# Kernel tuning notes

Measured on AMD Instinct MI355X. Metric: run time of the kernel, lower is better.

Reference implementation:

```python
import jax, jax.numpy as jnp
import numpy as np

B, M, D = 32768, 4096, 128


def setup_inputs() -> dict:
    key = jax.random.key(0)
    k1, k2 = jax.random.split(key)
    local_stats = jax.random.normal(k1, (B, D), dtype=jnp.float32)
    memory = jax.random.normal(k2, (M, D), dtype=jnp.float32)
    return {"local_stats": local_stats, "memory": memory}


def reference(local_stats, memory):
    # attention logits: [B, M] = x @ memory^T (unscaled single-head attention read)
    logits = jnp.einsum("bd,md->bm", local_stats, memory)
    attn = jax.nn.softmax(logits, axis=1)          # [B, M]
    global_stats = jnp.einsum("bm,md->bd", attn, memory)  # [B, D]
    return global_stats
```

## Files before the change

kernel.cpp:

```cpp
#include <hip/hip_runtime.h>
#include <hip/hip_bf16.h>
#include <stdint.h>


typedef float    f32x16 __attribute__((ext_vector_type(16)));
typedef _Float16 f16x8  __attribute__((ext_vector_type(8)));
typedef uint32_t u32;

#define AS1 __attribute__((address_space(1)))
#define AS3 __attribute__((address_space(3)))

#define D_DIM 128
#define B_ROWS 32768
#define TILE_HW 8192
#define HALF_TILES 64

#if __has_builtin(__builtin_amdgcn_exp2f)
#define EXP2F(x) __builtin_amdgcn_exp2f(x)
#else
#define EXP2F(x) exp2f(x)
#endif

__device__ __forceinline__ uint16_t f32_to_f16_bits(float x) {
    _Float16 h = (_Float16)x;
    uint16_t r; __builtin_memcpy(&r, &h, 2);
    return r;
}

__global__ void prep_frags(const float* __restrict__ mem,
                           uint16_t* __restrict__ kv) {
    int t = blockIdx.x * blockDim.x + threadIdx.x;
    int lane = t & 63;
    int fi = t >> 6;
    int f8 = fi & 7, mt = fi >> 3;
    size_t base = (size_t)mt * TILE_HW;
    {
        int m  = mt * 32 + (lane & 31);
        int d0 = f8 * 16 + (lane >> 5) * 8;
        const float* src = mem + (size_t)m * D_DIM + d0;
        #pragma unroll
        for (int e = 0; e < 8; ++e)
            kv[base + f8 * 512 + lane * 8 + e] = f32_to_f16_bits(src[e]);
    }
    {
        int dt = fi & 3, ks = (fi >> 2) & 1;
        int d  = dt * 32 + (lane & 31);
        int m0 = mt * 32 + ks * 16 + (lane >> 5) * 8;
        #pragma unroll
        for (int e = 0; e < 8; ++e)
            kv[base + 4096 + f8 * 512 + lane * 8 + e] =
                f32_to_f16_bits(mem[(size_t)(m0 + e) * D_DIM + d]);
    }
}


#define STAGE(t_, wb_) do {                                                   \
    const char* g_ = (const char*)(kv + (size_t)(tilebase + (t_)) * TILE_HW); \
    char* l_ = (char*)&sbuf[wb_][0];                                          \
    _Pragma("unroll")                                                         \
    for (int j_ = 0; j_ < 4; ++j_) {                                          \
        int ch_ = wave * 4 + j_;                                              \
        __builtin_amdgcn_global_load_lds(                                     \
            (const AS1 char*)(g_ + ch_ * 1024 + lane * 16),                   \
            (AS3 char*)(l_ + ch_ * 1024), 16, 0, 0);                          \
    }                                                                         \
} while (0)

#define MFMA_F16(a_, b_, c_) __builtin_amdgcn_mfma_f32_32x32x16_f16(a_, b_, c_, 0, 0, 0)

#define PSTORE_TILE(Ot_, t_) do {                                             \
    _Pragma("unroll")                                                         \
    for (int g_ = 0; g_ < 4; ++g_) {                                          \
        float4 v_ = { Ot_[4*g_+0], Ot_[4*g_+1], Ot_[4*g_+2], Ot_[4*g_+3] };   \
        int d_ = (t_) * 32 + 8 * g_ + 4 * hi32;                               \
        *(float4*)(prow + d_) = v_;                                           \
    }                                                                         \
} while (0)

__global__ __launch_bounds__(256, 2)
void attn_main(const float* __restrict__ qin,
               const uint16_t* __restrict__ kv,
               float* __restrict__ out0,
               float* __restrict__ pout1,
               float2* __restrict__ pml) {
    __shared__ uint16_t sbuf[2][TILE_HW];

    const int lane = threadIdx.x & 63;
    const int wave = threadIdx.x >> 6;
    const int half = blockIdx.x & 1;
    const int tilebase = half * HALF_TILES;
    const int q0   = (blockIdx.x >> 1) * 128 + wave * 32;
    const int qrow = q0 + (lane & 31);
    const int hi32 = lane >> 5;

    f16x8 qh[8];
    {
        const float LOG2E = 1.44269504088896340736f;
        #pragma unroll
        for (int kk = 0; kk < 8; ++kk) {
            const float* src = qin + (size_t)qrow * D_DIM + kk * 16 + hi32 * 8;
            float4 a = *(const float4*)(src);
            float4 b = *(const float4*)(src + 4);
            float xs[8] = {a.x, a.y, a.z, a.w, b.x, b.y, b.z, b.w};
            #pragma unroll
            for (int e = 0; e < 8; ++e)
                qh[kk][e] = (_Float16)(xs[e] * LOG2E);
        }
    }

    f32x16 O0, O1, O2, O3;
    #pragma unroll
    for (int i = 0; i < 16; ++i) { O0[i]=0.f; O1[i]=0.f; O2[i]=0.f; O3[i]=0.f; }
    float m_run = -1e30f, l_run = 0.f;

    STAGE(0, 0);
    __syncthreads();

    #pragma unroll 1
    for (int t = 0; t < HALF_TILES; ++t) {
        const int rb = t & 1;
        if (t + 1 < HALF_TILES) STAGE(t + 1, rb ^ 1);
        const uint16_t* bp = &sbuf[rb][0] + lane * 8;

        f16x8 kh[8];
        #pragma unroll
        for (int kk = 0; kk < 8; ++kk)
            kh[kk] = *(const f16x8*)(bp + kk * 512);

        f32x16 sA, sB;
        #pragma unroll
        for (int i = 0; i < 16; ++i) { sA[i] = 0.f; sB[i] = 0.f; }
        __builtin_amdgcn_s_setprio(1);
        sA = MFMA_F16(kh[0], qh[0], sA);
        sB = MFMA_F16(kh[1], qh[1], sB);
        sA = MFMA_F16(kh[2], qh[2], sA);
        sB = MFMA_F16(kh[3], qh[3], sB);
        sA = MFMA_F16(kh[4], qh[4], sA);
        sB = MFMA_F16(kh[5], qh[5], sB);
        sA = MFMA_F16(kh[6], qh[6], sA);
        sB = MFMA_F16(kh[7], qh[7], sB);
        __builtin_amdgcn_s_setprio(0);
        f32x16 s = sA + sB;

        {
            float a0=fmaxf(s[0],s[1]),  a1=fmaxf(s[2],s[3]);
            float a2=fmaxf(s[4],s[5]),  a3=fmaxf(s[6],s[7]);
            float a4=fmaxf(s[8],s[9]),  a5=fmaxf(s[10],s[11]);
            float a6=fmaxf(s[12],s[13]),a7=fmaxf(s[14],s[15]);
            float tmax = fmaxf(fmaxf(fmaxf(a0,a1),fmaxf(a2,a3)),
                               fmaxf(fmaxf(a4,a5),fmaxf(a6,a7)));
            tmax = fmaxf(tmax, __shfl_xor(tmax, 32));
            if (__any(tmax > m_run + 8.0f)) {
                float mn = fmaxf(m_run, tmax);
                float fr = EXP2F(m_run - mn);
                m_run = mn; l_run *= fr;
                #pragma unroll
                for (int r = 0; r < 16; ++r) {
                    O0[r] *= fr; O1[r] *= fr; O2[r] *= fr; O3[r] *= fr;
                }
            }
        }
        #pragma unroll
        for (int r = 0; r < 16; ++r) s[r] = EXP2F(s[r] - m_run);
        {
            float q0s=s[0]+s[1],  q1s=s[2]+s[3],  q2s=s[4]+s[5],  q3s=s[6]+s[7];
            float q4s=s[8]+s[9],  q5s=s[10]+s[11],q6s=s[12]+s[13],q7s=s[14]+s[15];
            l_run += ((q0s+q1s)+(q2s+q3s)) + ((q4s+q5s)+(q6s+q7s));
        }

        u32 c_[8];
        #pragma unroll
        for (int j = 0; j < 8; ++j)
            asm("v_cvt_pkrtz_f16_f32 %0, %1, %2"
                : "=v"(c_[j]) : "v"(s[2*j]), "v"(s[2*j+1]));
        asm("v_permlane32_swap_b32 %0, %1" : "+v"(c_[0]), "+v"(c_[2]));
        asm("v_permlane32_swap_b32 %0, %1" : "+v"(c_[1]), "+v"(c_[3]));
        asm("v_permlane32_swap_b32 %0, %1" : "+v"(c_[4]), "+v"(c_[6]));
        asm("v_permlane32_swap_b32 %0, %1" : "+v"(c_[5]), "+v"(c_[7]));
        f16x8 pf0, pf1;
        { u32 w[4] = {c_[0], c_[1], c_[2], c_[3]}; __builtin_memcpy(&pf0, w, 16); }
        { u32 w[4] = {c_[4], c_[5], c_[6], c_[7]}; __builtin_memcpy(&pf1, w, 16); }

        f16x8 vf[8];
        #pragma unroll
        for (int f = 0; f < 8; ++f)
            vf[f] = *(const f16x8*)(bp + 4096 + f * 512);
        __builtin_amdgcn_s_setprio(1);
        O0 = MFMA_F16(vf[0], pf0, O0);
        O1 = MFMA_F16(vf[1], pf0, O1);
        O2 = MFMA_F16(vf[2], pf0, O2);
        O3 = MFMA_F16(vf[3], pf0, O3);
        O0 = MFMA_F16(vf[4], pf1, O0);
        O1 = MFMA_F16(vf[5], pf1, O1);
        O2 = MFMA_F16(vf[6], pf1, O2);
        O3 = MFMA_F16(vf[7], pf1, O3);
        __builtin_amdgcn_s_setprio(0);
        __syncthreads();
    }

    l_run += __shfl_xor(l_run, 32);
    float* prow = (half == 0 ? out0 : pout1) + (size_t)qrow * D_DIM;
    PSTORE_TILE(O0, 0); PSTORE_TILE(O1, 1);
    PSTORE_TILE(O2, 2); PSTORE_TILE(O3, 3);
    if (lane < 32) {
        pml[(size_t)half * B_ROWS + qrow] = make_float2(m_run, l_run);
    }
}

__global__ __launch_bounds__(256)
void merge_halves(const float* __restrict__ pout1,
                  const float2* __restrict__ pml,
                  float* __restrict__ out) {
    int idx  = blockIdx.x * 256 + threadIdx.x;
    int row  = idx >> 5;
    int c4   = idx & 31;
    float2 a = pml[row];
    float2 b = pml[B_ROWS + row];
    float mn = fmaxf(a.x, b.x);
    float wa = EXP2F(a.x - mn);
    float wb = EXP2F(b.x - mn);
    float rinv = 1.0f / (a.y * wa + b.y * wb);
    float4* O = (float4*)(out + (size_t)row * D_DIM) + c4;
    const float4* P1 = (const float4*)(pout1 + (size_t)row * D_DIM) + c4;
    float4 p0 = *O, p1 = *P1;
    float4 v;
    v.x = (p0.x * wa + p1.x * wb) * rinv;
    v.y = (p0.y * wa + p1.y * wb) * rinv;
    v.z = (p0.z * wa + p1.z * wb) * rinv;
    v.w = (p0.w * wa + p1.w * wb) * rinv;
    *O = v;
}

extern "C" void kernel_launch(void* const* d_in, const int* in_sizes, int n_in,
                              void* d_out, int out_size, void* d_ws, size_t ws_size,
                              hipStream_t stream) {
    const float* local_stats = (const float*)d_in[0];
    const float* memory      = (const float*)d_in[1];
    float* out = (float*)d_out;

    uint16_t* kv   = (uint16_t*)d_ws;
    float*   pout1 = (float*)((char*)d_ws + 2 * 1024 * 1024);
    float2*  pml   = (float2*)((char*)pout1 + (size_t)B_ROWS * D_DIM * 4);

    prep_frags<<<256, 256, 0, stream>>>(memory, kv);
    attn_main<<<512, 256, 0, stream>>>(local_stats, kv, out, pout1, pml);
    merge_halves<<<4096, 256, 0, stream>>>(pout1, pml, out);
}
```

Before: 104.1 us.

## Process two KV tiles per iteration with a four-buffer LDS ring

New measurement: 101.4 us. 1.03x faster.

```diff
diff --git a/kernel.cpp b/kernel.cpp
--- a/kernel.cpp
+++ b/kernel.cpp
@@ -68,6 +68,73 @@
 
 #define MFMA_F16(a_, b_, c_) __builtin_amdgcn_mfma_f32_32x32x16_f16(a_, b_, c_, 0, 0, 0)
 
+#define QK(bp_, s_) do {                                                      \
+    f16x8 kh_[8];                                                             \
+    _Pragma("unroll")                                                         \
+    for (int kk_ = 0; kk_ < 8; ++kk_)                                         \
+        kh_[kk_] = *(const f16x8*)((bp_) + kk_ * 512);                        \
+    f32x16 sA_, sB_;                                                          \
+    _Pragma("unroll")                                                         \
+    for (int i_ = 0; i_ < 16; ++i_) { sA_[i_] = 0.f; sB_[i_] = 0.f; }         \
+    sA_ = MFMA_F16(kh_[0], qh[0], sA_);                                       \
+    sB_ = MFMA_F16(kh_[1], qh[1], sB_);                                       \
+    sA_ = MFMA_F16(kh_[2], qh[2], sA_);                                       \
+    sB_ = MFMA_F16(kh_[3], qh[3], sB_);                                       \
+    sA_ = MFMA_F16(kh_[4], qh[4], sA_);                                       \
+    sB_ = MFMA_F16(kh_[5], qh[5], sB_);                                       \
+    sA_ = MFMA_F16(kh_[6], qh[6], sA_);                                       \
+    sB_ = MFMA_F16(kh_[7], qh[7], sB_);                                       \
+    s_ = sA_ + sB_;                                                           \
+} while (0)
+
+#define SMX_PV(s_, bp_) do {                                                  \
+    float a0=fmaxf(s_[0],s_[1]),  a1=fmaxf(s_[2],s_[3]);                      \
+    float a2=fmaxf(s_[4],s_[5]),  a3=fmaxf(s_[6],s_[7]);                      \
+    float a4=fmaxf(s_[8],s_[9]),  a5=fmaxf(s_[10],s_[11]);                    \
+    float a6=fmaxf(s_[12],s_[13]),a7=fmaxf(s_[14],s_[15]);                    \
+    float tmax = fmaxf(fmaxf(fmaxf(a0,a1),fmaxf(a2,a3)),                      \
+                       fmaxf(fmaxf(a4,a5),fmaxf(a6,a7)));                     \
+    tmax = fmaxf(tmax, __shfl_xor(tmax, 32));                                 \
+    if (__any(tmax > m_run + 8.0f)) {                    \
+        float mn = fmaxf(m_run, tmax);                                        \
+        float fr = EXP2F(m_run - mn);                                         \
+        m_run = mn; l_run *= fr;                                              \
+        _Pragma("unroll")                                                     \
+        for (int r_ = 0; r_ < 16; ++r_) {                                     \
+            O0[r_] *= fr; O1[r_] *= fr; O2[r_] *= fr; O3[r_] *= fr;           \
+        }                                                                     \
+    }                                                                         \
+    _Pragma("unroll")                                                         \
+    for (int r_ = 0; r_ < 16; ++r_) s_[r_] = EXP2F(s_[r_] - m_run);           \
+    { float q0s=s_[0]+s_[1],  q1s=s_[2]+s_[3],  q2s=s_[4]+s_[5],  q3s=s_[6]+s_[7];   \
+      float q4s=s_[8]+s_[9],  q5s=s_[10]+s_[11],q6s=s_[12]+s_[13],q7s=s_[14]+s_[15]; \
+      l_run += ((q0s+q1s)+(q2s+q3s)) + ((q4s+q5s)+(q6s+q7s)); }               \
+    u32 c_[8];                                                                \
+    _Pragma("unroll")                                                         \
+    for (int j_ = 0; j_ < 8; ++j_)                                            \
+        asm("v_cvt_pkrtz_f16_f32 %0, %1, %2"                                  \
+            : "=v"(c_[j_]) : "v"(s_[2*j_]), "v"(s_[2*j_+1]));                 \
+    asm("v_permlane32_swap_b32 %0, %1" : "+v"(c_[0]), "+v"(c_[2]));           \
+    asm("v_permlane32_swap_b32 %0, %1" : "+v"(c_[1]), "+v"(c_[3]));           \
+    asm("v_permlane32_swap_b32 %0, %1" : "+v"(c_[4]), "+v"(c_[6]));           \
+    asm("v_permlane32_swap_b32 %0, %1" : "+v"(c_[5]), "+v"(c_[7]));           \
+    f16x8 pf0_, pf1_;                                                         \
+    { u32 w_[4] = {c_[0], c_[1], c_[2], c_[3]}; __builtin_memcpy(&pf0_, w_, 16); } \
+    { u32 w_[4] = {c_[4], c_[5], c_[6], c_[7]}; __builtin_memcpy(&pf1_, w_, 16); } \
+    f16x8 vf_[8];                                                             \
+    _Pragma("unroll")                                                         \
+    for (int f_ = 0; f_ < 8; ++f_)                                            \
+        vf_[f_] = *(const f16x8*)((bp_) + 4096 + f_ * 512);                   \
+    O0 = MFMA_F16(vf_[0], pf0_, O0);                                          \
+    O1 = MFMA_F16(vf_[1], pf0_, O1);                                          \
+    O2 = MFMA_F16(vf_[2], pf0_, O2);                                          \
+    O3 = MFMA_F16(vf_[3], pf0_, O3);                                          \
+    O0 = MFMA_F16(vf_[4], pf1_, O0);                                          \
+    O1 = MFMA_F16(vf_[5], pf1_, O1);                                          \
+    O2 = MFMA_F16(vf_[6], pf1_, O2);                                          \
+    O3 = MFMA_F16(vf_[7], pf1_, O3);                                          \
+} while (0)
+
 #define PSTORE_TILE(Ot_, t_) do {                                             \
     _Pragma("unroll")                                                         \
     for (int g_ = 0; g_ < 4; ++g_) {                                          \
@@ -83,7 +150,7 @@
                float* __restrict__ out0,
                float* __restrict__ pout1,
                float2* __restrict__ pml) {
-    __shared__ uint16_t sbuf[2][TILE_HW];
+    __shared__ uint16_t sbuf[4][TILE_HW];
 
     const int lane = threadIdx.x & 63;
     const int wave = threadIdx.x >> 6;
@@ -114,87 +181,21 @@
     float m_run = -1e30f, l_run = 0.f;
 
     STAGE(0, 0);
+    STAGE(1, 1);
     __syncthreads();
 
     #pragma unroll 1
-    for (int t = 0; t < HALF_TILES; ++t) {
-        const int rb = t & 1;
-        if (t + 1 < HALF_TILES) STAGE(t + 1, rb ^ 1);
-        const uint16_t* bp = &sbuf[rb][0] + lane * 8;
-
-        f16x8 kh[8];
-        #pragma unroll
-        for (int kk = 0; kk < 8; ++kk)
-            kh[kk] = *(const f16x8*)(bp + kk * 512);
-
-        f32x16 sA, sB;
-        #pragma unroll
-        for (int i = 0; i < 16; ++i) { sA[i] = 0.f; sB[i] = 0.f; }
-        __builtin_amdgcn_s_setprio(1);
-        sA = MFMA_F16(kh[0], qh[0], sA);
-        sB = MFMA_F16(kh[1], qh[1], sB);
-        sA = MFMA_F16(kh[2], qh[2], sA);
-        sB = MFMA_F16(kh[3], qh[3], sB);
-        sA = MFMA_F16(kh[4], qh[4], sA);
-        sB = MFMA_F16(kh[5], qh[5], sB);
-        sA = MFMA_F16(kh[6], qh[6], sA);
-        sB = MFMA_F16(kh[7], qh[7], sB);
-        __builtin_amdgcn_s_setprio(0);
-        f32x16 s = sA + sB;
-
-        {
-            float a0=fmaxf(s[0],s[1]),  a1=fmaxf(s[2],s[3]);
-            float a2=fmaxf(s[4],s[5]),  a3=fmaxf(s[6],s[7]);
-            float a4=fmaxf(s[8],s[9]),  a5=fmaxf(s[10],s[11]);
-            float a6=fmaxf(s[12],s[13]),a7=fmaxf(s[14],s[15]);
-            float tmax = fmaxf(fmaxf(fmaxf(a0,a1),fmaxf(a2,a3)),
-                               fmaxf(fmaxf(a4,a5),fmaxf(a6,a7)));
-            tmax = fmaxf(tmax, __shfl_xor(tmax, 32));
-            if (__any(tmax > m_run + 8.0f)) {
-                float mn = fmaxf(m_run, tmax);
-                float fr = EXP2F(m_run - mn);
-                m_run = mn; l_run *= fr;
-                #pragma unroll
-                for (int r = 0; r < 16; ++r) {
-                    O0[r] *= fr; O1[r] *= fr; O2[r] *= fr; O3[r] *= fr;
-                }
-            }
-        }
-        #pragma unroll
-        for (int r = 0; r < 16; ++r) s[r] = EXP2F(s[r] - m_run);
-        {
-            float q0s=s[0]+s[1],  q1s=s[2]+s[3],  q2s=s[4]+s[5],  q3s=s[6]+s[7];
-            float q4s=s[8]+s[9],  q5s=s[10]+s[11],q6s=s[12]+s[13],q7s=s[14]+s[15];
-            l_run += ((q0s+q1s)+(q2s+q3s)) + ((q4s+q5s)+(q6s+q7s));
-        }
-
-        u32 c_[8];
-        #pragma unroll
-        for (int j = 0; j < 8; ++j)
-            asm("v_cvt_pkrtz_f16_f32 %0, %1, %2"
-                : "=v"(c_[j]) : "v"(s[2*j]), "v"(s[2*j+1]));
-        asm("v_permlane32_swap_b32 %0, %1" : "+v"(c_[0]), "+v"(c_[2]));
-        asm("v_permlane32_swap_b32 %0, %1" : "+v"(c_[1]), "+v"(c_[3]));
-        asm("v_permlane32_swap_b32 %0, %1" : "+v"(c_[4]), "+v"(c_[6]));
-        asm("v_permlane32_swap_b32 %0, %1" : "+v"(c_[5]), "+v"(c_[7]));
-        f16x8 pf0, pf1;
-        { u32 w[4] = {c_[0], c_[1], c_[2], c_[3]}; __builtin_memcpy(&pf0, w, 16); }
-        { u32 w[4] = {c_[4], c_[5], c_[6], c_[7]}; __builtin_memcpy(&pf1, w, 16); }
-
-        f16x8 vf[8];
-        #pragma unroll
-        for (int f = 0; f < 8; ++f)
-            vf[f] = *(const f16x8*)(bp + 4096 + f * 512);
-        __builtin_amdgcn_s_setprio(1);
-        O0 = MFMA_F16(vf[0], pf0, O0);
-        O1 = MFMA_F16(vf[1], pf0, O1);
-        O2 = MFMA_F16(vf[2], pf0, O2);
-        O3 = MFMA_F16(vf[3], pf0, O3);
-        O0 = MFMA_F16(vf[4], pf1, O0);
-        O1 = MFMA_F16(vf[5], pf1, O1);
-        O2 = MFMA_F16(vf[6], pf1, O2);
-        O3 = MFMA_F16(vf[7], pf1, O3);
-        __builtin_amdgcn_s_setprio(0);
+    for (int t = 0; t < HALF_TILES; t += 2) {
+        if (t + 2 < HALF_TILES) STAGE(t + 2, (t + 2) & 3);
+        if (t + 3 < HALF_TILES) STAGE(t + 3, (t + 3) & 3);
+        const uint16_t* bp0 = &sbuf[t & 3][0] + lane * 8;
+        const uint16_t* bp1 = &sbuf[(t + 1) & 3][0] + lane * 8;
+
+        f32x16 s0, s1;
+        QK(bp0, s0);
+        QK(bp1, s1);
+        SMX_PV(s0, bp0);
+        SMX_PV(s1, bp1);
         __syncthreads();
     }
 
```
